# Performance work log

Measured on AMD Instinct MI355X. Metric: run time of the kernel, lower is better.

The kernel has to match this reference:

```python
import jax, jax.numpy as jnp
import numpy as np

N_NODES = 50000
N_EDGES = 500000
N_REL = 8
D = 128        # input_dim
A_DIM = 64     # attention_dim
D_OUT = 128    # output_dim


def setup_inputs() -> dict:
    key = jax.random.key(0)
    ks = jax.random.split(key, 10)
    h = jax.random.normal(ks[0], (N_NODES, D), jnp.float32)
    # relation gate tables: [R, 2*D, D]; first D rows act on dst (subject), last D on src (object)
    relations = jax.random.normal(ks[1], (N_REL, 2 * D, D), jnp.float32) * 0.05
    rel_attention = jax.random.normal(ks[2], (N_REL, A_DIM), jnp.float32) * 0.05
    W_a = jax.random.normal(ks[3], (A_DIM, 2 * D), jnp.float32) * 0.05
    b_a = jnp.zeros((A_DIM,), jnp.float32)
    W_lin = jax.random.normal(ks[4], (D_OUT, 2 * D), jnp.float32) * 0.05
    b_lin = jnp.zeros((D_OUT,), jnp.float32)
    src = jax.random.randint(ks[5], (N_EDGES,), 0, N_NODES, dtype=jnp.int32)
    dst = jax.random.randint(ks[6], (N_EDGES,), 0, N_NODES, dtype=jnp.int32)
    etype = jax.random.randint(ks[7], (N_EDGES,), 0, N_REL, dtype=jnp.int32)
    return {"h": h, "relations": relations, "rel_attention": rel_attention,
            "W_a": W_a, "b_a": b_a, "W_lin": W_lin, "b_lin": b_lin,
            "src": src, "dst": dst, "etype": etype}


def reference(h, relations, rel_attention, W_a, b_a, W_lin, b_lin, src, dst, etype):
    d = h.shape[-1]
    # --- gates: relation-indexed gather_mm (concat gate type) ---
    # Project every node through every relation once (R is small), then gather per edge.
    proj_dst = jnp.einsum('nd,rde->rne', h, relations[:, :d, :])   # [R, N, D] subject/dst side
    proj_src = jnp.einsum('nd,rde->rne', h, relations[:, d:, :])   # [R, N, D] object/src side
    gate = jax.nn.sigmoid(proj_dst[etype, dst] + proj_src[etype, src])  # [E, D]

    src_h = h[src]   # [E, D]
    dst_h = h[dst]   # [E, D]

    # --- gatv2 attention (predicates are zeroed in the module -> rel_attention[0]) ---
    a = jax.nn.leaky_relu(jnp.concatenate([dst_h, src_h], axis=-1) @ W_a.T + b_a)  # [E, A]
    score = (rel_attention[0] * a).sum(-1)  # [E]

    # --- edge_softmax over destination-node segments ---
    smax = jax.ops.segment_max(score, dst, num_segments=N_NODES)
    ex = jnp.exp(score - smax[dst])
    denom = jax.ops.segment_sum(ex, dst, num_segments=N_NODES)
    attn = ex / denom[dst]  # [E]

    # --- message = u_mul_e(h, attn*gate), reduce = sum over dst ---
    msg = src_h * (attn[:, None] * gate)                 # [E, D]
    h_N = jax.ops.segment_sum(msg, dst, num_segments=N_NODES)  # [N, D]

    # --- graphsage aggregate: LeakyReLU(W [h ; h_N] + b) ---
    out = jax.nn.leaky_relu(jnp.concatenate([h, h_N], axis=-1) @ W_lin.T + b_lin)
    return out
```

## Files before the change

kernel.cpp:

```cpp
#include <hip/hip_runtime.h>
#include <cstdint>
#include <cstddef>

constexpr int NNODES = 50000;
constexpr int NEDGES = 500000;
constexpr int NRELS  = 8;
constexpr int DIM    = 128;
constexpr int ADIM   = 64;
constexpr int TWOD   = 256;
constexpr int EPB    = 64;
constexpr float SLOPE = 0.01f;

constexpr int XPITCH = TWOD + 8;
constexpr int SPAD = NEDGES + 1024;

typedef __attribute__((ext_vector_type(8))) short short8;
typedef __attribute__((ext_vector_type(4))) float floatx4;

__device__ __forceinline__ unsigned short f2bf(float f) {
    unsigned u = __float_as_uint(f);
    unsigned r = u + 0x7FFFu + ((u >> 16) & 1u);
    return (unsigned short)(r >> 16);
}
__device__ __forceinline__ float bf2f(unsigned short b) {
    return __uint_as_float(((unsigned)b) << 16);
}
__device__ __forceinline__ float sigmoid_fast(float x) {
    return __builtin_amdgcn_rcpf(1.0f + __expf(-x));
}

__global__ void k_init(int* __restrict__ histD, int* __restrict__ cursorD,
                       int* __restrict__ cnts) {
    int i = blockIdx.x * blockDim.x + threadIdx.x;
    int stride = gridDim.x * blockDim.x;
    for (int idx = i; idx < NNODES; idx += stride) { histD[idx] = 0; cursorD[idx] = 0; }
    if (i < 16) cnts[i] = 0;
}

__global__ __launch_bounds__(256) void k_prep(const float* __restrict__ rel,
                                              const float* __restrict__ W_lin,
                                              const float* __restrict__ W_a,
                                              unsigned short* __restrict__ relT,
                                              unsigned short* __restrict__ Wl,
                                              unsigned short* __restrict__ Wa16) {
    __shared__ float ls[64][65];
    int b = blockIdx.x, t = threadIdx.x;
    if (b < 64) {
        int r = b >> 3, tile = b & 7;
        int d0 = (tile >> 1) * 64, o0 = (tile & 1) * 64;
        const float* rp = rel + ((size_t)r * TWOD + d0) * DIM + o0;
#pragma unroll
        for (int u = 0; u < 16; u++) {
            int v = u * 256 + t;
            int j = v & 63, i = v >> 6;
            ls[i][j] = rp[(size_t)i * DIM + j];
        }
        __syncthreads();
        unsigned short* wp = relT + ((size_t)r * DIM + o0) * TWOD + d0;
#pragma unroll
        for (int u = 0; u < 16; u++) {
            int v = u * 256 + t;
            int ii = v & 63, jj = v >> 6;
            wp[(size_t)jj * TWOD + ii] = f2bf(ls[ii][jj]);
        }
    } else {
        int idx = (b - 64) * 256 + t;
        if (idx < DIM * TWOD) {
            Wl[idx] = f2bf(W_lin[idx]);
        } else {
            int j = idx - DIM * TWOD;
            if (j < ADIM * TWOD) Wa16[j] = f2bf(W_a[j]);
        }
    }
}

__global__ void k_h16(const float* __restrict__ h, unsigned short* __restrict__ h16) {
    int i = blockIdx.x * 256 + threadIdx.x;
    if (i < NNODES * DIM / 8) {
        const float4* hp = (const float4*)(h + (size_t)i * 8);
        float4 a = hp[0], b = hp[1];
        union { unsigned short us[8]; short8 s8; } pk;
        pk.us[0] = f2bf(a.x); pk.us[1] = f2bf(a.y); pk.us[2] = f2bf(a.z); pk.us[3] = f2bf(a.w);
        pk.us[4] = f2bf(b.x); pk.us[5] = f2bf(b.y); pk.us[6] = f2bf(b.z); pk.us[7] = f2bf(b.w);
        *(short8*)&h16[(size_t)i * 8] = pk.s8;
    }
}

__global__ void k_hist2(const int* __restrict__ ety, const int* __restrict__ dst,
                        int* __restrict__ cnt, int* __restrict__ histD) {
    __shared__ int hist[NRELS];
    int t = threadIdx.x;
    if (t < NRELS) hist[t] = 0;
    __syncthreads();
    int e = blockIdx.x * 256 + t;
    if (e < NEDGES) {
        atomicAdd(&hist[ety[e]], 1);
        atomicAdd(&histD[dst[e]], 1);
    }
    __syncthreads();
    if (t < NRELS && hist[t] > 0) atomicAdd(&cnt[t], hist[t]);
}

__global__ __launch_bounds__(1024) void k_scan(const int* __restrict__ histD,
                                               int* __restrict__ row_ptr,
                                               const int* __restrict__ cnt,
                                               int* __restrict__ offs,
                                               uint2* __restrict__ sMeta) {
    __shared__ int ls[1024];
    __shared__ int s_offs[NRELS + 1];
    __shared__ int s_cnt[NRELS];
    const int t = threadIdx.x;
    const int CH = (NNODES + 1023) / 1024;
    const int base = t * CH;
    int s = 0;
    for (int j = 0; j < CH; j++) { int i = base + j; if (i < NNODES) s += histD[i]; }
    ls[t] = s;
    __syncthreads();
    for (int off = 1; off < 1024; off <<= 1) {
        int v = (t >= off) ? ls[t - off] : 0;
        __syncthreads();
        ls[t] += v;
        __syncthreads();
    }
    int run = (t == 0) ? 0 : ls[t - 1];
    for (int j = 0; j < CH; j++) {
        int i = base + j;
        if (i < NNODES) { row_ptr[i] = run; run += histD[i]; }
    }
    if (t == 1023) row_ptr[NNODES] = ls[1023];
    if (t == 0) {
        int off = 0;
        for (int r = 0; r < NRELS; r++) {
            offs[r] = off; s_offs[r] = off; s_cnt[r] = cnt[r];
            off += ((cnt[r] + EPB - 1) / EPB) * EPB;
        }
        s_offs[NRELS] = off;
    }
    __syncthreads();
#pragma unroll
    for (int r = 0; r < NRELS; r++) {
        int s0 = s_offs[r] + s_cnt[r];
        int e0 = s_offs[r + 1 > NRELS ? NRELS : r + 1];
        for (int idx = s0 + t; idx < e0; idx += 1024) sMeta[idx] = make_uint2(0xFFFFFFFFu, 0u);
    }
    for (int idx = s_offs[NRELS] + t; idx < SPAD; idx += 1024)
        sMeta[idx] = make_uint2(0xFFFFFFFFu, 0u);
}

__global__ void k_escatter(const int* __restrict__ ety, const int* __restrict__ src,
                           const int* __restrict__ dst, const int* __restrict__ row_ptr,
                           const int* __restrict__ offs,
                           int* __restrict__ cursorD, int* __restrict__ cursorE,
                           uint2* __restrict__ sMeta) {
    __shared__ int hist[NRELS];
    __shared__ int basew[NRELS];
    int t = threadIdx.x;
    if (t < NRELS) hist[t] = 0;
    __syncthreads();
    int e = blockIdx.x * 256 + t;
    int r = -1, rank = 0, sn = 0, dn = 0;
    if (e < NEDGES) {
        r = ety[e]; sn = src[e]; dn = dst[e];
        rank = atomicAdd(&hist[r], 1);
    }
    __syncthreads();
    if (t < NRELS && hist[t] > 0) basew[t] = atomicAdd(&cursorE[t], hist[t]);
    __syncthreads();
    if (e < NEDGES) {
        int s = offs[r] + basew[r] + rank;
        int pos = row_ptr[dn] + atomicAdd(&cursorD[dn], 1);
        sMeta[s] = make_uint2((unsigned)sn | ((unsigned)dn << 16), (unsigned)pos);
    }
}

__global__ __launch_bounds__(256, 5) void k_gate_msg(
    const unsigned short* __restrict__ h16, const unsigned short* __restrict__ relT,
    const unsigned short* __restrict__ Wa16,
    const uint2* __restrict__ sMeta, const float* __restrict__ b_a,
    const float* __restrict__ ratt, const int* __restrict__ offs,
    unsigned short* __restrict__ msgbuf, float* __restrict__ scoreP) {
    __shared__ unsigned short Xs[EPB * 256];

    const int t = threadIdx.x;
    const int base = blockIdx.x * EPB;
    const int lane = t & 63;
    const int wave = t >> 6;

    uint2 sm = sMeta[base + lane];
    const unsigned smx = sm.x;
    const unsigned smy = sm.y;

    if (__shfl((int)smx, 0) == -1) return;

    int r = 0;
#pragma unroll
    for (int i = 1; i < NRELS; i++) if (base >= offs[i]) r = i;

#pragma unroll
    for (int u = 0; u < 8; u++) {
        int i = u * 8 + (t >> 5);
        int c = t & 31;
        unsigned x = (unsigned)__shfl((int)smx, i);
        int node = (x == 0xFFFFFFFFu) ? 0 : ((c < 16) ? (int)(x >> 16) : (int)(x & 0xFFFFu));
        *(short8*)&Xs[i * 256 + ((c ^ (i & 7)) << 3)] =
            *(const short8*)&h16[(size_t)node * DIM + (c & 15) * 8];
    }

    const int q = lane >> 4;
    const int l16 = lane & 15;
    const int o16 = wave * 16 + l16;

    const unsigned short* bp0 = relT + ((size_t)r * DIM + (wave * 2 + 0) * 16 + l16) * TWOD + q * 8;
    const unsigned short* bp1 = relT + ((size_t)r * DIM + (wave * 2 + 1) * 16 + l16) * TWOD + q * 8;
    const unsigned short* wb  = Wa16 + (size_t)o16 * TWOD + q * 8;

    __syncthreads();

    floatx4 acc[4][2];
    floatx4 accS[4];
#pragma unroll
    for (int m = 0; m < 4; m++) {
        acc[m][0] = (floatx4)(0.0f);
        acc[m][1] = (floatx4)(0.0f);
        accS[m] = (floatx4)(0.0f);
    }

#pragma unroll
    for (int ks = 0; ks < 8; ks++) {
        short8 B0 = *(const short8*)(bp0 + ks * 32);
        short8 B1 = *(const short8*)(bp1 + ks * 32);
        short8 BS = *(const short8*)(wb + ks * 32);
        short8 Af[4];
#pragma unroll
        for (int m = 0; m < 4; m++) {
            int row = m * 16 + l16;
            Af[m] = *(const short8*)&Xs[row * 256 + ((((ks * 4) + q) ^ (l16 & 7)) << 3)];
        }
#pragma unroll
        for (int m = 0; m < 4; m++) {
            acc[m][0] = __builtin_amdgcn_mfma_f32_16x16x32_bf16(Af[m], B0, acc[m][0], 0, 0, 0);
            acc[m][1] = __builtin_amdgcn_mfma_f32_16x16x32_bf16(Af[m], B1, acc[m][1], 0, 0, 0);
            accS[m]   = __builtin_amdgcn_mfma_f32_16x16x32_bf16(Af[m], BS, accS[m], 0, 0, 0);
        }
    }

    __syncthreads();

#pragma unroll
    for (int m = 0; m < 4; m++) {
        int ib = m * 16 + q * 4;
#pragma unroll
        for (int nn = 0; nn < 2; nn++) {
            int o = (wave * 2 + nn) * 16 + l16;
            int uS = 16 + (o >> 3), uD = o >> 3, ofs = o & 7;
#pragma unroll
            for (int rg = 0; rg < 4; rg++) {
                int i = ib + rg;
                float g = sigmoid_fast(acc[m][nn][rg]);
                float sh = bf2f(Xs[i * 256 + ((uS ^ (i & 7)) << 3) + ofs]);
                Xs[i * 256 + ((uD ^ (i & 7)) << 3) + ofs] = f2bf(sh * g);
            }
        }
    }
    __syncthreads();

    {
        float ba = b_a[o16];
        float ra = ratt[o16];
#pragma unroll
        for (int m = 0; m < 4; m++) {
#pragma unroll
            for (int rg = 0; rg < 4; rg++) {
                float v = accS[m][rg] + ba;
                v = v > 0.0f ? v : SLOPE * v;
                v *= ra;
#pragma unroll
                for (int off = 8; off > 0; off >>= 1) v += __shfl_xor(v, off, 16);
                if (l16 == 0) ((float*)&Xs[(m * 16 + q * 4 + rg) * 256 + 128])[wave] = v;
            }
        }
    }

#pragma unroll
    for (int u = 0; u < 4; u++) {
        int i = u * 16 + (t >> 4);
        int c = t & 15;
        unsigned x = (unsigned)__shfl((int)smx, i);
        unsigned pos = (unsigned)__shfl((int)smy, i);
        if (x == 0xFFFFFFFFu) continue;
        short8 val = *(const short8*)&Xs[i * 256 + ((c ^ (i & 7)) << 3)];
        *(short8*)&msgbuf[(size_t)pos * DIM + c * 8] = val;
    }
    __syncthreads();

    if (t < EPB && smx != 0xFFFFFFFFu) {
        const float* sw = (const float*)&Xs[t * 256 + 128];
        scoreP[smy] = sw[0] + sw[1] + sw[2] + sw[3];
    }
}

__global__ __launch_bounds__(256) void k_aggr(const unsigned short* __restrict__ msgbuf,
                                              const float* __restrict__ scoreP,
                                              const int* __restrict__ row_ptr,
                                              unsigned short* __restrict__ hN16) {
    int n = blockIdx.x * 4 + (threadIdx.x >> 6);
    int lane = threadIdx.x & 63;
    if (n >= NNODES) return;
    int p0 = row_ptr[n], p1 = row_ptr[n + 1];
    float a0 = 0.0f, a1 = 0.0f;
    if (p0 < p1) {
        float mx = -3.0e38f;
        for (int p = p0 + lane; p < p1; p += 64) mx = fmaxf(mx, scoreP[p]);
#pragma unroll
        for (int off = 32; off > 0; off >>= 1) mx = fmaxf(mx, __shfl_xor(mx, off));
        float sum = 0.0f;
        for (int p = p0 + lane; p < p1; p += 64) sum += __expf(scoreP[p] - mx);
#pragma unroll
        for (int off = 32; off > 0; off >>= 1) sum += __shfl_xor(sum, off);
        int p = p0;
        const unsigned short* mb = msgbuf + (size_t)lane * 2;
        for (; p + 4 <= p1; p += 4) {
            float w0 = __expf(scoreP[p + 0] - mx);
            float w1 = __expf(scoreP[p + 1] - mx);
            float w2 = __expf(scoreP[p + 2] - mx);
            float w3 = __expf(scoreP[p + 3] - mx);
            unsigned v0 = *(const unsigned*)&mb[(size_t)(p + 0) * DIM];
            unsigned v1 = *(const unsigned*)&mb[(size_t)(p + 1) * DIM];
            unsigned v2 = *(const unsigned*)&mb[(size_t)(p + 2) * DIM];
            unsigned v3 = *(const unsigned*)&mb[(size_t)(p + 3) * DIM];
            a0 = fmaf(w0, bf2f((unsigned short)(v0 & 0xFFFFu)), a0);
            a1 = fmaf(w0, bf2f((unsigned short)(v0 >> 16)), a1);
            a0 = fmaf(w1, bf2f((unsigned short)(v1 & 0xFFFFu)), a0);
            a1 = fmaf(w1, bf2f((unsigned short)(v1 >> 16)), a1);
            a0 = fmaf(w2, bf2f((unsigned short)(v2 & 0xFFFFu)), a0);
            a1 = fmaf(w2, bf2f((unsigned short)(v2 >> 16)), a1);
            a0 = fmaf(w3, bf2f((unsigned short)(v3 & 0xFFFFu)), a0);
            a1 = fmaf(w3, bf2f((unsigned short)(v3 >> 16)), a1);
        }
        for (; p < p1; p++) {
            float w = __expf(scoreP[p] - mx);
            unsigned v = *(const unsigned*)&mb[(size_t)p * DIM];
            a0 = fmaf(w, bf2f((unsigned short)(v & 0xFFFFu)), a0);
            a1 = fmaf(w, bf2f((unsigned short)(v >> 16)), a1);
        }
        float inv = __builtin_amdgcn_rcpf(sum);
        a0 *= inv; a1 *= inv;
    }
    unsigned o = (unsigned)f2bf(a0) | ((unsigned)f2bf(a1) << 16);
    *(unsigned*)&hN16[(size_t)n * DIM + lane * 2] = o;
}

__global__ __launch_bounds__(256) void k_out(const unsigned short* __restrict__ h16,
                                             const unsigned short* __restrict__ hN16,
                                             const unsigned short* __restrict__ Wl,
                                             const float* __restrict__ b_lin,
                                             float* __restrict__ out) {
    __shared__ unsigned short Xs[EPB * XPITCH];
    const int t = threadIdx.x;
    const int nb = blockIdx.x * 64;

#pragma unroll
    for (int u = 0; u < 8; u++) {
        int v = u * 256 + t;
        int i = v >> 5;
        int c = v & 31;
        int n = nb + i;
        if (n >= NNODES) n = NNODES - 1;
        const unsigned short* srcp = (c < 16) ? h16 : hN16;
        *(short8*)&Xs[i * XPITCH + c * 8] = *(const short8*)&srcp[(size_t)n * DIM + (c & 15) * 8];
    }

    const int wave = t >> 6;
    const int lane = t & 63;
    const int q = lane >> 4;
    const int l16 = lane & 15;

    short8 Bf[2][8];
#pragma unroll
    for (int nn = 0; nn < 2; nn++) {
        int o = (wave * 2 + nn) * 16 + l16;
        const unsigned short* bp = Wl + (size_t)o * TWOD + q * 8;
#pragma unroll
        for (int ks = 0; ks < 8; ks++) Bf[nn][ks] = *(const short8*)(bp + ks * 32);
    }

    __syncthreads();

    floatx4 acc[4][2];
#pragma unroll
    for (int m = 0; m < 4; m++)
#pragma unroll
        for (int nn = 0; nn < 2; nn++) acc[m][nn] = (floatx4)(0.0f);

#pragma unroll
    for (int ks = 0; ks < 8; ks++) {
        short8 Af[4];
        const unsigned short* xb = &Xs[l16 * XPITCH + ks * 32 + q * 8];
#pragma unroll
        for (int m = 0; m < 4; m++) Af[m] = *(const short8*)(xb + m * 16 * XPITCH);
#pragma unroll
        for (int m = 0; m < 4; m++)
#pragma unroll
            for (int nn = 0; nn < 2; nn++)
                acc[m][nn] = __builtin_amdgcn_mfma_f32_16x16x32_bf16(Af[m], Bf[nn][ks], acc[m][nn], 0, 0, 0);
    }

#pragma unroll
    for (int m = 0; m < 4; m++) {
        int ib = m * 16 + q * 4;
#pragma unroll
        for (int nn = 0; nn < 2; nn++) {
            int o = (wave * 2 + nn) * 16 + l16;
            float bl = b_lin[o];
#pragma unroll
            for (int rg = 0; rg < 4; rg++) {
                int n = nb + ib + rg;
                if (n < NNODES) {
                    float val = acc[m][nn][rg] + bl;
                    val = val > 0.0f ? val : SLOPE * val;
                    out[(size_t)n * DIM + o] = val;
                }
            }
        }
    }
}

extern "C" void kernel_launch(void* const* d_in, const int* in_sizes, int n_in,
                              void* d_out, int out_size, void* d_ws, size_t ws_size,
                              hipStream_t stream) {
    const float* h     = (const float*)d_in[0];
    const float* rel   = (const float*)d_in[1];
    const float* ratt  = (const float*)d_in[2];
    const float* W_a   = (const float*)d_in[3];
    const float* b_a   = (const float*)d_in[4];
    const float* W_lin = (const float*)d_in[5];
    const float* b_lin = (const float*)d_in[6];
    const int* src = (const int*)d_in[7];
    const int* dst = (const int*)d_in[8];
    const int* ety = (const int*)d_in[9];
    float* out = (float*)d_out;

    float* scoreP = (float*)d_ws;
    unsigned short* h16  = (unsigned short*)(scoreP + NEDGES);
    unsigned short* hN16 = h16 + (size_t)NNODES * DIM;
    unsigned short* relT = hN16 + (size_t)NNODES * DIM;
    unsigned short* Wl   = relT + (size_t)NRELS * DIM * TWOD;
    unsigned short* Wa16 = Wl + (size_t)DIM * TWOD;
    uint2* sMeta = (uint2*)(Wa16 + (size_t)ADIM * TWOD);
    int* row_ptr = (int*)(sMeta + SPAD);
    int* histD   = row_ptr + (NNODES + 1);
    int* cursorD = histD + NNODES;
    int* cnts    = cursorD + NNODES;
    int* offs    = cnts + 16;
    unsigned short* msgbuf = (unsigned short*)(((uintptr_t)(offs + 8) + 255) & ~(uintptr_t)255);

    k_init<<<256, 256, 0, stream>>>(histD, cursorD, cnts);
    k_prep<<<64 + (DIM * TWOD + ADIM * TWOD + 255) / 256, 256, 0, stream>>>(
        rel, W_lin, W_a, relT, Wl, Wa16);
    k_h16<<<(NNODES * DIM / 8 + 255) / 256, 256, 0, stream>>>(h, h16);
    k_hist2<<<(NEDGES + 255) / 256, 256, 0, stream>>>(ety, dst, cnts, histD);
    k_scan<<<1, 1024, 0, stream>>>(histD, row_ptr, cnts, offs, sMeta);
    k_escatter<<<(NEDGES + 255) / 256, 256, 0, stream>>>(
        ety, src, dst, row_ptr, offs, cursorD, cnts + 8, sMeta);
    k_gate_msg<<<(NEDGES + 8 * EPB + EPB - 1) / EPB, 256, 0, stream>>>(
        h16, relT, Wa16, sMeta, b_a, ratt, offs, msgbuf, scoreP);
    k_aggr<<<(NNODES + 3) / 4, 256, 0, stream>>>(msgbuf, scoreP, row_ptr, hN16);
    k_out<<<(NNODES + 63) / 64, 256, 0, stream>>>(h16, hN16, Wl, b_lin, out);
}
```

Before: 459.1 us.

## Gather node features directly into LDS and prefetch relation weights early

The per-edge node feature gather in k_gate_msg now uses global_load_lds, so data goes straight into the swizzled LDS tile instead of through registers. Edge metadata is staged in shared arrays rather than broadcast with shuffles. The first relation-weight fragment is prefetched into registers before the barrier. Attention scores go to a separate shared array, which removes one barrier. This aims to hide gather latency and cut VGPR traffic, in exchange for more register pressure, lowering the occupancy hint from 5 to 4.

Result: no change. 454.5 us (-1.0%).

```diff
diff --git a/kernel.cpp b/kernel.cpp
--- a/kernel.cpp
+++ b/kernel.cpp
@@ -27,6 +27,12 @@
 }
 __device__ __forceinline__ float sigmoid_fast(float x) {
     return __builtin_amdgcn_rcpf(1.0f + __expf(-x));
+}
+
+typedef const __attribute__((address_space(1))) void* gas_ptr;
+typedef __attribute__((address_space(3))) void* las_ptr;
+__device__ __forceinline__ void gload_lds16(const void* g, void* l) {
+    __builtin_amdgcn_global_load_lds((gas_ptr)g, (las_ptr)l, 16, 0, 0);
 }
 
 __global__ void k_init(int* __restrict__ histD, int* __restrict__ cursorD,
@@ -173,24 +179,34 @@
     }
 }
 
-__global__ __launch_bounds__(256, 5) void k_gate_msg(
+__global__ __launch_bounds__(256, 4) void k_gate_msg(
     const unsigned short* __restrict__ h16, const unsigned short* __restrict__ relT,
     const unsigned short* __restrict__ Wa16,
     const uint2* __restrict__ sMeta, const float* __restrict__ b_a,
     const float* __restrict__ ratt, const int* __restrict__ offs,
     unsigned short* __restrict__ msgbuf, float* __restrict__ scoreP) {
     __shared__ unsigned short Xs[EPB * 256];
+    __shared__ int srcn_s[EPB];
+    __shared__ int dstn_s[EPB];
+    __shared__ int pos_s[EPB];
+    __shared__ int val_s[EPB];
+    __shared__ float scoreW[EPB][4];
 
     const int t = threadIdx.x;
     const int base = blockIdx.x * EPB;
     const int lane = t & 63;
     const int wave = t >> 6;
 
-    uint2 sm = sMeta[base + lane];
-    const unsigned smx = sm.x;
-    const unsigned smy = sm.y;
-
-    if (__shfl((int)smx, 0) == -1) return;
+    if (t < EPB) {
+        uint2 m2 = sMeta[base + t];
+        int valid = (m2.x != 0xFFFFFFFFu);
+        val_s[t] = valid;
+        srcn_s[t] = valid ? (int)(m2.x & 0xFFFFu) : 0;
+        dstn_s[t] = valid ? (int)(m2.x >> 16) : 0;
+        pos_s[t] = valid ? (int)m2.y : 0;
+    }
+    __syncthreads();
+    if (!val_s[0]) return;
 
     int r = 0;
 #pragma unroll
@@ -198,12 +214,11 @@
 
 #pragma unroll
     for (int u = 0; u < 8; u++) {
-        int i = u * 8 + (t >> 5);
-        int c = t & 31;
-        unsigned x = (unsigned)__shfl((int)smx, i);
-        int node = (x == 0xFFFFFFFFu) ? 0 : ((c < 16) ? (int)(x >> 16) : (int)(x & 0xFFFFu));
-        *(short8*)&Xs[i * 256 + ((c ^ (i & 7)) << 3)] =
-            *(const short8*)&h16[(size_t)node * DIM + (c & 15) * 8];
+        int j = wave * 8 + u;
+        int row = j * 2 + (lane >> 5);
+        int lu = (lane & 31) ^ (row & 7);
+        int node = (lu < 16) ? dstn_s[row] : srcn_s[row];
+        gload_lds16(&h16[(size_t)node * DIM + (lu & 15) * 8], &Xs[j * 512]);
     }
 
     const int q = lane >> 4;
@@ -213,6 +228,12 @@
     const unsigned short* bp0 = relT + ((size_t)r * DIM + (wave * 2 + 0) * 16 + l16) * TWOD + q * 8;
     const unsigned short* bp1 = relT + ((size_t)r * DIM + (wave * 2 + 1) * 16 + l16) * TWOD + q * 8;
     const unsigned short* wb  = Wa16 + (size_t)o16 * TWOD + q * 8;
+
+    short8 B0p[8];
+#pragma unroll
+    for (int ks = 0; ks < 8; ks++) B0p[ks] = *(const short8*)(bp0 + ks * 32);
+#pragma unroll
+    for (int ks = 0; ks < 8; ks++) asm volatile("" :: "v"(B0p[ks]));
 
     __syncthreads();
 
@@ -227,7 +248,7 @@
 
 #pragma unroll
     for (int ks = 0; ks < 8; ks++) {
-        short8 B0 = *(const short8*)(bp0 + ks * 32);
+        short8 B0 = B0p[ks];
         short8 B1 = *(const short8*)(bp1 + ks * 32);
         short8 BS = *(const short8*)(wb + ks * 32);
         short8 Af[4];
@@ -245,6 +266,23 @@
     }
 
     __syncthreads();
+
+    {
+        float ba = b_a[o16];
+        float ra = ratt[o16];
+#pragma unroll
+        for (int m = 0; m < 4; m++) {
+#pragma unroll
+            for (int rg = 0; rg < 4; rg++) {
+                float v = accS[m][rg] + ba;
+                v = v > 0.0f ? v : SLOPE * v;
+                v *= ra;
+#pragma unroll
+                for (int off = 8; off > 0; off >>= 1) v += __shfl_xor(v, off, 16);
+                if (l16 == 0) scoreW[m * 16 + q * 4 + rg][wave] = v;
+            }
+        }
+    }
 
 #pragma unroll
     for (int m = 0; m < 4; m++) {
@@ -264,38 +302,17 @@
     }
     __syncthreads();
 
-    {
-        float ba = b_a[o16];
-        float ra = ratt[o16];
-#pragma unroll
-        for (int m = 0; m < 4; m++) {
-#pragma unroll
-            for (int rg = 0; rg < 4; rg++) {
-                float v = accS[m][rg] + ba;
-                v = v > 0.0f ? v : SLOPE * v;
-                v *= ra;
-#pragma unroll
-                for (int off = 8; off > 0; off >>= 1) v += __shfl_xor(v, off, 16);
-                if (l16 == 0) ((float*)&Xs[(m * 16 + q * 4 + rg) * 256 + 128])[wave] = v;
-            }
-        }
-    }
-
 #pragma unroll
     for (int u = 0; u < 4; u++) {
-        int i = u * 16 + (t >> 4);
-        int c = t & 15;
-        unsigned x = (unsigned)__shfl((int)smx, i);
-        unsigned pos = (unsigned)__shfl((int)smy, i);
-        if (x == 0xFFFFFFFFu) continue;
+        int v = u * 256 + t;
+        int i = v >> 4;
+        int c = v & 15;
+        if (!val_s[i]) continue;
         short8 val = *(const short8*)&Xs[i * 256 + ((c ^ (i & 7)) << 3)];
-        *(short8*)&msgbuf[(size_t)pos * DIM + c * 8] = val;
-    }
-    __syncthreads();
-
-    if (t < EPB && smx != 0xFFFFFFFFu) {
-        const float* sw = (const float*)&Xs[t * 256 + 128];
-        scoreP[smy] = sw[0] + sw[1] + sw[2] + sw[3];
+        *(short8*)&msgbuf[(size_t)pos_s[i] * DIM + c * 8] = val;
+    }
+    if (t < EPB && val_s[t]) {
+        scoreP[pos_s[t]] = scoreW[t][0] + scoreW[t][1] + scoreW[t][2] + scoreW[t][3];
     }
 }
 
```

## Make gate/message kernel persistent with register-prefetched gathers of next edge group

Applied to the files above, without the earlier changes.

Turns k_gate_msg into a persistent kernel over a fixed grid of 1024 blocks. Each block loops over edge groups and prefetches the next group's node features and metadata into registers while computing the current one. The shared tile switches from an XOR swizzle to a padded pitch, scores get a separate shared array, and the cursorD zeroing moves from k_init into k_scan. The aim is to hide gather latency behind MFMA work and cut block launch overhead. In exchange it uses more registers (occupancy hint drops from 5 to 4) and adds extra barriers per iteration.

New measurement: 546.0 us. +18.9%, slower.

```diff
diff --git a/kernel.cpp b/kernel.cpp
--- a/kernel.cpp
+++ b/kernel.cpp
@@ -13,6 +13,8 @@
 
 constexpr int XPITCH = TWOD + 8;
 constexpr int SPAD = NEDGES + 1024;
+constexpr int NGRP = (NEDGES + 8 * EPB + EPB - 1) / EPB;
+constexpr int GGRID = 1024;
 
 typedef __attribute__((ext_vector_type(8))) short short8;
 typedef __attribute__((ext_vector_type(4))) float floatx4;
@@ -28,12 +30,15 @@
 __device__ __forceinline__ float sigmoid_fast(float x) {
     return __builtin_amdgcn_rcpf(1.0f + __expf(-x));
 }
-
-__global__ void k_init(int* __restrict__ histD, int* __restrict__ cursorD,
-                       int* __restrict__ cnts) {
+__device__ __forceinline__ void barrier_lgkm() {
+    asm volatile("s_waitcnt lgkmcnt(0)" ::: "memory");
+    __builtin_amdgcn_s_barrier();
+}
+
+__global__ void k_init(int* __restrict__ histD, int* __restrict__ cnts) {
     int i = blockIdx.x * blockDim.x + threadIdx.x;
     int stride = gridDim.x * blockDim.x;
-    for (int idx = i; idx < NNODES; idx += stride) { histD[idx] = 0; cursorD[idx] = 0; }
+    for (int idx = i; idx < NNODES; idx += stride) histD[idx] = 0;
     if (i < 16) cnts[i] = 0;
 }
 
@@ -103,6 +108,7 @@
 
 __global__ __launch_bounds__(1024) void k_scan(const int* __restrict__ histD,
                                                int* __restrict__ row_ptr,
+                                               int* __restrict__ cursorD,
                                                const int* __restrict__ cnt,
                                                int* __restrict__ offs,
                                                uint2* __restrict__ sMeta) {
@@ -125,7 +131,7 @@
     int run = (t == 0) ? 0 : ls[t - 1];
     for (int j = 0; j < CH; j++) {
         int i = base + j;
-        if (i < NNODES) { row_ptr[i] = run; run += histD[i]; }
+        if (i < NNODES) { row_ptr[i] = run; cursorD[i] = 0; run += histD[i]; }
     }
     if (t == 1023) row_ptr[NNODES] = ls[1023];
     if (t == 0) {
@@ -173,100 +179,124 @@
     }
 }
 
-__global__ __launch_bounds__(256, 5) void k_gate_msg(
+__global__ __launch_bounds__(256, 4) void k_gate_msg(
     const unsigned short* __restrict__ h16, const unsigned short* __restrict__ relT,
     const unsigned short* __restrict__ Wa16,
     const uint2* __restrict__ sMeta, const float* __restrict__ b_a,
     const float* __restrict__ ratt, const int* __restrict__ offs,
     unsigned short* __restrict__ msgbuf, float* __restrict__ scoreP) {
-    __shared__ unsigned short Xs[EPB * 256];
+    __shared__ unsigned short Xs[EPB * XPITCH];
+    __shared__ int pos_s[2][EPB];
+    __shared__ int val_s[2][EPB];
+    __shared__ float scoreW[EPB][4];
 
     const int t = threadIdx.x;
-    const int base = blockIdx.x * EPB;
     const int lane = t & 63;
     const int wave = t >> 6;
-
-    uint2 sm = sMeta[base + lane];
-    const unsigned smx = sm.x;
-    const unsigned smy = sm.y;
-
-    if (__shfl((int)smx, 0) == -1) return;
-
-    int r = 0;
-#pragma unroll
-    for (int i = 1; i < NRELS; i++) if (base >= offs[i]) r = i;
-
-#pragma unroll
-    for (int u = 0; u < 8; u++) {
-        int i = u * 8 + (t >> 5);
-        int c = t & 31;
-        unsigned x = (unsigned)__shfl((int)smx, i);
-        int node = (x == 0xFFFFFFFFu) ? 0 : ((c < 16) ? (int)(x >> 16) : (int)(x & 0xFFFFu));
-        *(short8*)&Xs[i * 256 + ((c ^ (i & 7)) << 3)] =
-            *(const short8*)&h16[(size_t)node * DIM + (c & 15) * 8];
-    }
-
     const int q = lane >> 4;
     const int l16 = lane & 15;
     const int o16 = wave * 16 + l16;
-
-    const unsigned short* bp0 = relT + ((size_t)r * DIM + (wave * 2 + 0) * 16 + l16) * TWOD + q * 8;
-    const unsigned short* bp1 = relT + ((size_t)r * DIM + (wave * 2 + 1) * 16 + l16) * TWOD + q * 8;
-    const unsigned short* wb  = Wa16 + (size_t)o16 * TWOD + q * 8;
-
-    __syncthreads();
-
-    floatx4 acc[4][2];
-    floatx4 accS[4];
-#pragma unroll
-    for (int m = 0; m < 4; m++) {
-        acc[m][0] = (floatx4)(0.0f);
-        acc[m][1] = (floatx4)(0.0f);
-        accS[m] = (floatx4)(0.0f);
-    }
-
-#pragma unroll
-    for (int ks = 0; ks < 8; ks++) {
-        short8 B0 = *(const short8*)(bp0 + ks * 32);
-        short8 B1 = *(const short8*)(bp1 + ks * 32);
-        short8 BS = *(const short8*)(wb + ks * 32);
-        short8 Af[4];
+    const int i0 = t >> 5;
+    const int c  = t & 31;
+    const int ch = (c & 15) * 8;
+
+    int g = (int)blockIdx.x;
+    int nxt = g + GGRID; if (nxt >= NGRP) nxt = g;
+
+    int offv[NRELS];
+#pragma unroll
+    for (int i = 0; i < NRELS; i++) offv[i] = offs[i];
+
+    float ba = b_a[o16];
+    float ra = ratt[o16];
+
+    short8 Gs[8];
+    {
+        unsigned mg0[8];
+#pragma unroll
+        for (int u = 0; u < 8; u++) mg0[u] = sMeta[(size_t)g * EPB + u * 8 + i0].x;
+#pragma unroll
+        for (int u = 0; u < 8; u++) {
+            unsigned x = mg0[u];
+            int node = (x == 0xFFFFFFFFu) ? 0 : ((c < 16) ? (int)(x >> 16) : (int)(x & 0xFFFFu));
+            Gs[u] = *(const short8*)&h16[(size_t)node * DIM + ch];
+        }
+    }
+    unsigned MG[8];
+#pragma unroll
+    for (int u = 0; u < 8; u++) MG[u] = sMeta[(size_t)nxt * EPB + u * 8 + i0].x;
+    uint2 MU = make_uint2(0xFFFFFFFFu, 0u);
+    if (t < EPB) {
+        uint2 m0 = sMeta[(size_t)g * EPB + t];
+        int valid = (m0.x != 0xFFFFFFFFu);
+        val_s[0][t] = valid;
+        pos_s[0][t] = valid ? (int)m0.y : 0;
+        MU = sMeta[(size_t)nxt * EPB + t];
+    }
+    int p = 0;
+
+    while (true) {
+#pragma unroll
+        for (int u = 0; u < 8; u++)
+            *(short8*)&Xs[(u * 8 + i0) * XPITCH + c * 8] = Gs[u];
+
+#pragma unroll
+        for (int u = 0; u < 8; u++) {
+            unsigned x = MG[u];
+            int node = (x == 0xFFFFFFFFu) ? 0 : ((c < 16) ? (int)(x >> 16) : (int)(x & 0xFFFFu));
+            Gs[u] = *(const short8*)&h16[(size_t)node * DIM + ch];
+        }
+        int nn2 = nxt + GGRID; if (nn2 >= NGRP) nn2 = nxt;
+#pragma unroll
+        for (int u = 0; u < 8; u++) MG[u] = sMeta[(size_t)nn2 * EPB + u * 8 + i0].x;
+        if (t < EPB) {
+            int valid = (MU.x != 0xFFFFFFFFu);
+            val_s[p ^ 1][t] = valid;
+            pos_s[p ^ 1][t] = valid ? (int)MU.y : 0;
+            MU = sMeta[(size_t)nn2 * EPB + t];
+        }
+
+        barrier_lgkm();
+
+        int r = 0;
+        {
+            int gE = g * EPB;
+#pragma unroll
+            for (int i = 1; i < NRELS; i++) if (gE >= offv[i]) r = i;
+        }
+        const unsigned short* bp0 = relT + (size_t)r * (DIM * TWOD)
+            + ((size_t)((wave * 2) * 16 + l16)) * TWOD + q * 8;
+        const unsigned short* bp1 = bp0 + (size_t)16 * TWOD;
+        const unsigned short* wb  = Wa16 + (size_t)o16 * TWOD + q * 8;
+
+        floatx4 acc[4][2];
+        floatx4 accS[4];
 #pragma unroll
         for (int m = 0; m < 4; m++) {
-            int row = m * 16 + l16;
-            Af[m] = *(const short8*)&Xs[row * 256 + ((((ks * 4) + q) ^ (l16 & 7)) << 3)];
-        }
-#pragma unroll
-        for (int m = 0; m < 4; m++) {
-            acc[m][0] = __builtin_amdgcn_mfma_f32_16x16x32_bf16(Af[m], B0, acc[m][0], 0, 0, 0);
-            acc[m][1] = __builtin_amdgcn_mfma_f32_16x16x32_bf16(Af[m], B1, acc[m][1], 0, 0, 0);
-            accS[m]   = __builtin_amdgcn_mfma_f32_16x16x32_bf16(Af[m], BS, accS[m], 0, 0, 0);
-        }
-    }
-
-    __syncthreads();
-
-#pragma unroll
-    for (int m = 0; m < 4; m++) {
-        int ib = m * 16 + q * 4;
-#pragma unroll
-        for (int nn = 0; nn < 2; nn++) {
-            int o = (wave * 2 + nn) * 16 + l16;
-            int uS = 16 + (o >> 3), uD = o >> 3, ofs = o & 7;
-#pragma unroll
-            for (int rg = 0; rg < 4; rg++) {
-                int i = ib + rg;
-                float g = sigmoid_fast(acc[m][nn][rg]);
-                float sh = bf2f(Xs[i * 256 + ((uS ^ (i & 7)) << 3) + ofs]);
-                Xs[i * 256 + ((uD ^ (i & 7)) << 3) + ofs] = f2bf(sh * g);
+            acc[m][0] = (floatx4)(0.0f);
+            acc[m][1] = (floatx4)(0.0f);
+            accS[m] = (floatx4)(0.0f);
+        }
+
+#pragma unroll
+        for (int ks = 0; ks < 8; ks++) {
+            short8 B0 = *(const short8*)(bp0 + ks * 32);
+            short8 B1 = *(const short8*)(bp1 + ks * 32);
+            short8 BS = *(const short8*)(wb + ks * 32);
+            short8 Af[4];
+            const unsigned short* xb = &Xs[l16 * XPITCH + ks * 32 + q * 8];
+#pragma unroll
+            for (int m = 0; m < 4; m++) Af[m] = *(const short8*)(xb + m * 16 * XPITCH);
+#pragma unroll
+            for (int m = 0; m < 4; m++) {
+                acc[m][0] = __builtin_amdgcn_mfma_f32_16x16x32_bf16(Af[m], B0, acc[m][0], 0, 0, 0);
+                acc[m][1] = __builtin_amdgcn_mfma_f32_16x16x32_bf16(Af[m], B1, acc[m][1], 0, 0, 0);
+                accS[m]   = __builtin_amdgcn_mfma_f32_16x16x32_bf16(Af[m], BS, accS[m], 0, 0, 0);
             }
         }
-    }
-    __syncthreads();
-
-    {
-        float ba = b_a[o16];
-        float ra = ratt[o16];
+
+        barrier_lgkm();
+
 #pragma unroll
         for (int m = 0; m < 4; m++) {
 #pragma unroll
@@ -276,26 +306,48 @@
                 v *= ra;
 #pragma unroll
                 for (int off = 8; off > 0; off >>= 1) v += __shfl_xor(v, off, 16);
-                if (l16 == 0) ((float*)&Xs[(m * 16 + q * 4 + rg) * 256 + 128])[wave] = v;
+                if (l16 == 0) scoreW[m * 16 + q * 4 + rg][wave] = v;
             }
         }
-    }
-
-#pragma unroll
-    for (int u = 0; u < 4; u++) {
-        int i = u * 16 + (t >> 4);
-        int c = t & 15;
-        unsigned x = (unsigned)__shfl((int)smx, i);
-        unsigned pos = (unsigned)__shfl((int)smy, i);
-        if (x == 0xFFFFFFFFu) continue;
-        short8 val = *(const short8*)&Xs[i * 256 + ((c ^ (i & 7)) << 3)];
-        *(short8*)&msgbuf[(size_t)pos * DIM + c * 8] = val;
-    }
-    __syncthreads();
-
-    if (t < EPB && smx != 0xFFFFFFFFu) {
-        const float* sw = (const float*)&Xs[t * 256 + 128];
-        scoreP[smy] = sw[0] + sw[1] + sw[2] + sw[3];
+
+#pragma unroll
+        for (int m = 0; m < 4; m++) {
+            int ib = m * 16 + q * 4;
+#pragma unroll
+            for (int nn = 0; nn < 2; nn++) {
+                int o = (wave * 2 + nn) * 16 + l16;
+#pragma unroll
+                for (int rg = 0; rg < 4; rg++) {
+                    int i = ib + rg;
+                    float gt = sigmoid_fast(acc[m][nn][rg]);
+                    float sh = bf2f(Xs[i * XPITCH + DIM + o]);
+                    Xs[i * XPITCH + o] = f2bf(sh * gt);
+                }
+            }
+        }
+
+        barrier_lgkm();
+
+#pragma unroll
+        for (int u = 0; u < 4; u++) {
+            int v = u * 256 + t;
+            int i = v >> 4;
+            int cc = v & 15;
+            if (val_s[p][i]) {
+                short8 val = *(const short8*)&Xs[i * XPITCH + cc * 8];
+                *(short8*)&msgbuf[(size_t)pos_s[p][i] * DIM + cc * 8] = val;
+            }
+        }
+        if (t < EPB && val_s[p][t]) {
+            scoreP[pos_s[p][t]] = scoreW[t][0] + scoreW[t][1] + scoreW[t][2] + scoreW[t][3];
+        }
+
+        g += GGRID;
+        if (g >= NGRP) break;
+        nxt = g + GGRID; if (nxt >= NGRP) nxt = g;
+        p ^= 1;
+
+        barrier_lgkm();
     }
 }
 
@@ -454,15 +506,15 @@
     int* offs    = cnts + 16;
     unsigned short* msgbuf = (unsigned short*)(((uintptr_t)(offs + 8) + 255) & ~(uintptr_t)255);
 
-    k_init<<<256, 256, 0, stream>>>(histD, cursorD, cnts);
+    k_init<<<196, 256, 0, stream>>>(histD, cnts);
     k_prep<<<64 + (DIM * TWOD + ADIM * TWOD + 255) / 256, 256, 0, stream>>>(
         rel, W_lin, W_a, relT, Wl, Wa16);
     k_h16<<<(NNODES * DIM / 8 + 255) / 256, 256, 0, stream>>>(h, h16);
     k_hist2<<<(NEDGES + 255) / 256, 256, 0, stream>>>(ety, dst, cnts, histD);
-    k_scan<<<1, 1024, 0, stream>>>(histD, row_ptr, cnts, offs, sMeta);
+    k_scan<<<1, 1024, 0, stream>>>(histD, row_ptr, cursorD, cnts, offs, sMeta);
     k_escatter<<<(NEDGES + 255) / 256, 256, 0, stream>>>(
         ety, src, dst, row_ptr, offs, cursorD, cnts + 8, sMeta);
-    k_gate_msg<<<(NEDGES + 8 * EPB + EPB - 1) / EPB, 256, 0, stream>>>(
+    k_gate_msg<<<GGRID, 256, 0, stream>>>(
         h16, relT, Wa16, sMeta, b_a, ratt, offs, msgbuf, scoreP);
     k_aggr<<<(NNODES + 3) / 4, 256, 0, stream>>>(msgbuf, scoreP, row_ptr, hN16);
     k_out<<<(NNODES + 63) / 64, 256, 0, stream>>>(h16, hN16, Wl, b_lin, out);
```
